# Optimization experiments

Hardware: AMD Instinct MI355X
Metric: run time of the kernel (lower is better)

The kernel has to match this reference:

```python
import jax, jax.numpy as jnp
import numpy as np

NUM_CLUSTERS = 64
DIM = 512
ALPHA = 100.0
EPS = 1e-12  # torch F.normalize eps


def setup_inputs() -> dict:
    key = jax.random.key(0)
    k1, k2 = jax.random.split(key)
    x1 = jax.random.normal(k1, (30, DIM, 28, 28), dtype=jnp.float32)
    centroids = jax.random.uniform(k2, (NUM_CLUSTERS, DIM), dtype=jnp.float32)
    # _init_params: conv weight = 2*alpha*centroids (1x1 conv), bias = -alpha*||centroid||
    conv_w = 2.0 * ALPHA * centroids
    conv_b = -ALPHA * jnp.linalg.norm(centroids, axis=1)
    return {"x1": x1, "centroids": centroids, "conv_w": conv_w, "conv_b": conv_b}


def _l2norm(v, axis):
    n = jnp.sqrt(jnp.sum(v * v, axis=axis, keepdims=True))
    return v / jnp.maximum(n, EPS)


def reference(x1, centroids, conv_w, conv_b):
    T, C, H, W = x1.shape
    K, D = centroids.shape
    x = x1.reshape(T, C, H * W)            # [T, C, N]
    x = _l2norm(x, axis=1)                 # normalize_input: L2 over channel dim
    # 1x1 conv == matmul over channels: logits [T, K, N]
    logits = jnp.einsum('kc,tcn->tkn', conv_w, x) + conv_b[None, :, None]
    a = jax.nn.softmax(logits, axis=1)     # soft assignment over clusters
    # vlad[t,k,c] = sum_n a[t,k,n]*(x[t,c,n] - centroids[k,c])
    # rewritten as two small matmuls, avoiding the [K,C,N] residual tensor
    vlad = jnp.einsum('tkn,tcn->tkc', a, x) - a.sum(axis=-1)[:, :, None] * centroids[None]
    vlad = _l2norm(vlad, axis=2)           # intra-normalization over feature dim
    v = vlad.reshape(T, K * D)
    v = _l2norm(v, axis=1)                 # global L2 normalization
    return v.sum(axis=0, keepdims=True)    # [1, K*D] accumulated over 30 timesteps
```

## Files before the change

kernel.cpp:

```cpp
#include <hip/hip_runtime.h>
#include <math.h>

#define T_ 30
#define C_ 512
#define N_ 784
#define NA_ 800
#define QP 36
#define EPSV 1e-12f

typedef __attribute__((ext_vector_type(8))) short bf16x8;
typedef __attribute__((ext_vector_type(4))) float f32x4;

__device__ __forceinline__ unsigned short f2bf(float f) {
    union { float f; unsigned int u; } v; v.f = f;
    unsigned int r = (v.u + 0x7FFFu + ((v.u >> 16) & 1u)) >> 16;
    return (unsigned short)r;
}
__device__ __forceinline__ float bf2f(unsigned short h) {
    union { unsigned int u; float f; } v; v.u = ((unsigned int)h) << 16;
    return v.f;
}

__global__ void k_prep(const float* __restrict__ w, unsigned short* __restrict__ wh,
                       unsigned short* __restrict__ wl) {
    int idx = blockIdx.x * 256 + threadIdx.x;
    float v = w[idx];
    unsigned short h = f2bf(v);
    wh[idx] = h;
    wl[idx] = f2bf(v - bf2f(h));
}

__global__ __launch_bounds__(256, 4) void k_assign(
    const float* __restrict__ x, const unsigned short* __restrict__ wh,
    const unsigned short* __restrict__ wl, const float* __restrict__ b,
    unsigned short* __restrict__ aT, float* __restrict__ asum)
{
    __shared__ __align__(16) char smem[4 * 32 * QP * 2 * 2];
    unsigned short* xh = (unsigned short*)smem;
    unsigned short* xl = xh + 4 * 32 * QP;
    float* red = (float*)smem;
    __shared__ float ssq[4][32];

    int t = blockIdx.y, n0 = blockIdx.x * 32;
    int tid = threadIdx.x;
    int w = tid >> 6, L = tid & 63, lid = L & 15, quad = L >> 4;
    int cbase = w * 128;
    int nseg = (L & 7) * 4;
    int crow = L >> 3;

    int ncol = n0 + nseg;
    if (ncol > 780) ncol = 780;
    const float* xb = x + (size_t)t * C_ * N_ + ncol;
    unsigned short* shh = xh + w * 32 * QP;
    unsigned short* shl = xl + w * 32 * QP;
    const unsigned short* wha = wh + (size_t)lid * C_ + cbase + quad * 8;
    const unsigned short* wla = wl + (size_t)lid * C_ + cbase + quad * 8;

    float bk = b[L];
    float ss0 = 0.f, ss1 = 0.f, ss2 = 0.f, ss3 = 0.f;
    f32x4 acc[4][2];
    #pragma unroll
    for (int mt = 0; mt < 4; ++mt)
        #pragma unroll
        for (int nt = 0; nt < 2; ++nt)
            #pragma unroll
            for (int r = 0; r < 4; ++r) acc[mt][nt][r] = 0.f;

    #pragma unroll
    for (int qtr = 0; qtr < 4; ++qtr) {
        float4 q[4];
        #pragma unroll
        for (int p = 0; p < 4; ++p)
            q[p] = *reinterpret_cast<const float4*>(
                xb + (size_t)(cbase + qtr * 32 + p * 8 + crow) * N_);
        #pragma unroll
        for (int p = 0; p < 4; ++p) {
            int cl = p * 8 + crow;
            float vv[4] = {q[p].x, q[p].y, q[p].z, q[p].w};
            ss0 = fmaf(vv[0], vv[0], ss0); ss1 = fmaf(vv[1], vv[1], ss1);
            ss2 = fmaf(vv[2], vv[2], ss2); ss3 = fmaf(vv[3], vv[3], ss3);
            #pragma unroll
            for (int j = 0; j < 4; ++j) {
                unsigned short h = f2bf(vv[j]);
                shh[(nseg + j) * QP + cl] = h;
                shl[(nseg + j) * QP + cl] = f2bf(vv[j] - bf2f(h));
            }
        }
        int so = quad * 8;
        bf16x8 bh0 = *reinterpret_cast<const bf16x8*>(&shh[lid * QP + so]);
        bf16x8 bl0 = *reinterpret_cast<const bf16x8*>(&shl[lid * QP + so]);
        bf16x8 bh1 = *reinterpret_cast<const bf16x8*>(&shh[(16 + lid) * QP + so]);
        bf16x8 bl1 = *reinterpret_cast<const bf16x8*>(&shl[(16 + lid) * QP + so]);
        int cg = qtr * 32;
        #pragma unroll
        for (int mt = 0; mt < 4; ++mt) {
            bf16x8 ah = *reinterpret_cast<const bf16x8*>(
                wha + (size_t)mt * 16 * C_ + cg);
            bf16x8 al = *reinterpret_cast<const bf16x8*>(
                wla + (size_t)mt * 16 * C_ + cg);
            acc[mt][0] = __builtin_amdgcn_mfma_f32_16x16x32_bf16(ah, bh0, acc[mt][0], 0, 0, 0);
            acc[mt][0] = __builtin_amdgcn_mfma_f32_16x16x32_bf16(al, bh0, acc[mt][0], 0, 0, 0);
            acc[mt][0] = __builtin_amdgcn_mfma_f32_16x16x32_bf16(ah, bl0, acc[mt][0], 0, 0, 0);
            acc[mt][1] = __builtin_amdgcn_mfma_f32_16x16x32_bf16(ah, bh1, acc[mt][1], 0, 0, 0);
            acc[mt][1] = __builtin_amdgcn_mfma_f32_16x16x32_bf16(al, bh1, acc[mt][1], 0, 0, 0);
            acc[mt][1] = __builtin_amdgcn_mfma_f32_16x16x32_bf16(ah, bl1, acc[mt][1], 0, 0, 0);
        }
    }
    #pragma unroll
    for (int m = 8; m <= 32; m <<= 1) {
        ss0 += __shfl_xor(ss0, m, 64); ss1 += __shfl_xor(ss1, m, 64);
        ss2 += __shfl_xor(ss2, m, 64); ss3 += __shfl_xor(ss3, m, 64);
    }
    if (L < 8) {
        ssq[w][L * 4 + 0] = ss0; ssq[w][L * 4 + 1] = ss1;
        ssq[w][L * 4 + 2] = ss2; ssq[w][L * 4 + 3] = ss3;
    }
    __syncthreads();

    float asl = 0.f;
    #pragma unroll
    for (int ph = 0; ph < 2; ++ph) {
        {
            float* rp = red + w * (16 * 68);
            #pragma unroll
            for (int mt = 0; mt < 4; ++mt)
                *reinterpret_cast<f32x4*>(&rp[lid * 68 + mt * 16 + quad * 4]) = acc[mt][ph];
        }
        __syncthreads();
        float vv[4], iv[4];
        #pragma unroll
        for (int i = 0; i < 4; ++i) {
            int nl = ph * 16 + w * 4 + i;
            float s = ssq[0][nl] + ssq[1][nl] + ssq[2][nl] + ssq[3][nl];
            iv[i] = 1.0f / fmaxf(sqrtf(s), EPSV);
            int nr = w * 4 + i;
            float v = red[0 * 1088 + nr * 68 + L] + red[1 * 1088 + nr * 68 + L]
                    + red[2 * 1088 + nr * 68 + L] + red[3 * 1088 + nr * 68 + L];
            vv[i] = fmaf(v, iv[i], bk);
        }
        float mx[4] = {vv[0], vv[1], vv[2], vv[3]};
        #pragma unroll
        for (int m = 1; m <= 32; m <<= 1) {
            #pragma unroll
            for (int i = 0; i < 4; ++i) mx[i] = fmaxf(mx[i], __shfl_xor(mx[i], m, 64));
        }
        float e[4], se[4];
        #pragma unroll
        for (int i = 0; i < 4; ++i) { e[i] = __expf(vv[i] - mx[i]); se[i] = e[i]; }
        #pragma unroll
        for (int m = 1; m <= 32; m <<= 1) {
            #pragma unroll
            for (int i = 0; i < 4; ++i) se[i] += __shfl_xor(se[i], m, 64);
        }
        unsigned short av[4];
        #pragma unroll
        for (int i = 0; i < 4; ++i) {
            bool valid = (n0 + ph * 16 + w * 4 + i) < N_;
            float a = e[i] / se[i];
            av[i] = valid ? f2bf(a * iv[i]) : (unsigned short)0;
            asl += valid ? a : 0.f;
        }
        ushort4 st; st.x = av[0]; st.y = av[1]; st.z = av[2]; st.w = av[3];
        *reinterpret_cast<ushort4*>(
            aT + ((size_t)t * 64 + L) * NA_ + n0 + ph * 16 + w * 4) = st;
        if (ph == 0) __syncthreads();
    }
    atomicAdd(&asum[t * 64 + L], asl);
}

__global__ __launch_bounds__(256, 4) void k_vlad(
    const float* __restrict__ x, const unsigned short* __restrict__ aT,
    const float* __restrict__ asum, const float* __restrict__ cent,
    float* __restrict__ vlad, float* __restrict__ g2)
{
    __shared__ float red[4][16 * 36];
    int t = blockIdx.z, kh = blockIdx.y, c0 = blockIdx.x * 16;
    int tid = threadIdx.x;
    int w = tid >> 6, L = tid & 63, lid = L & 15, quad = L >> 4;

    f32x4 acc[2];
    #pragma unroll
    for (int mt = 0; mt < 2; ++mt)
        #pragma unroll
        for (int r = 0; r < 4; ++r) acc[mt][r] = 0.f;

    const float* xrow = x + ((size_t)t * C_ + c0 + lid) * N_;
    const unsigned short* a0 = aT + ((size_t)t * 64 + kh * 32 + lid) * NA_;

    int k_loc = tid >> 3, j8 = tid & 7, ce = j8 * 2;
    int kg = kh * 32 + k_loc;
    float as = asum[t * 64 + kg];
    float2 cv = *reinterpret_cast<const float2*>(cent + kg * C_ + c0 + ce);

    int nb = w * 32 + quad * 8;
    int nc = nb > 776 ? 776 : nb;
    float4 x0c = *reinterpret_cast<const float4*>(xrow + nc);
    float4 x1c = *reinterpret_cast<const float4*>(xrow + nc + 4);
    bf16x8 f0 = *reinterpret_cast<const bf16x8*>(a0 + nb);
    bf16x8 f1 = *reinterpret_cast<const bf16x8*>(a0 + 16 * NA_ + nb);

    for (int s = w; s < 25; s += 4) {
        int sn = s + 4;
        float4 x0n = x0c, x1n = x1c;
        bf16x8 g0 = f0, g1 = f1;
        if (sn < 25) {
            int nb2 = sn * 32 + quad * 8;
            int nc2 = nb2 > 776 ? 776 : nb2;
            x0n = *reinterpret_cast<const float4*>(xrow + nc2);
            x1n = *reinterpret_cast<const float4*>(xrow + nc2 + 4);
            g0  = *reinterpret_cast<const bf16x8*>(a0 + nb2);
            g1  = *reinterpret_cast<const bf16x8*>(a0 + 16 * NA_ + nb2);
        }
        bf16x8 bb;
        bb[0] = (short)f2bf(x0c.x); bb[1] = (short)f2bf(x0c.y);
        bb[2] = (short)f2bf(x0c.z); bb[3] = (short)f2bf(x0c.w);
        bb[4] = (short)f2bf(x1c.x); bb[5] = (short)f2bf(x1c.y);
        bb[6] = (short)f2bf(x1c.z); bb[7] = (short)f2bf(x1c.w);
        acc[0] = __builtin_amdgcn_mfma_f32_16x16x32_bf16(f0, bb, acc[0], 0, 0, 0);
        acc[1] = __builtin_amdgcn_mfma_f32_16x16x32_bf16(f1, bb, acc[1], 0, 0, 0);
        x0c = x0n; x1c = x1n; f0 = g0; f1 = g1;
    }
    {
        float* rp = &red[w][0];
        #pragma unroll
        for (int mt = 0; mt < 2; ++mt)
            *reinterpret_cast<f32x4*>(&rp[lid * 36 + mt * 16 + quad * 4]) = acc[mt];
    }
    __syncthreads();

    float2 vout;
    float s2 = 0.f;
    #pragma unroll
    for (int j = 0; j < 2; ++j) {
        int cc = ce + j;
        float v = red[0][cc * 36 + k_loc] + red[1][cc * 36 + k_loc]
                + red[2][cc * 36 + k_loc] + red[3][cc * 36 + k_loc];
        v -= as * ((const float*)&cv)[j];
        ((float*)&vout)[j] = v;
        s2 = fmaf(v, v, s2);
    }
    *reinterpret_cast<float2*>(vlad + ((size_t)t * 64 + kg) * C_ + c0 + ce) = vout;
    s2 += __shfl_xor(s2, 1, 64);
    s2 += __shfl_xor(s2, 2, 64);
    s2 += __shfl_xor(s2, 4, 64);
    if (j8 == 0) atomicAdd(&g2[t * 64 + kg], s2);
}

__global__ __launch_bounds__(256) void k_out(
    const float* __restrict__ vlad, const float* __restrict__ g2,
    float* __restrict__ out)
{
    __shared__ float intr[1920];
    __shared__ float gl[1920];
    __shared__ float sinv[T_];
    __shared__ float part[256];
    int tid = threadIdx.x;
    for (int i = tid; i < 1920; i += 256) {
        float s = g2[i];
        gl[i] = s;
        intr[i] = 1.0f / fmaxf(sqrtf(s), EPSV);
    }
    __syncthreads();
    if (tid < T_) {
        float s = 0.f;
        #pragma unroll 8
        for (int k = 0; k < 64; ++k) {
            float iv = intr[tid * 64 + k];
            s += gl[tid * 64 + k] * iv * iv;
        }
        sinv[tid] = 1.0f / fmaxf(sqrtf(s), EPSV);
    }
    __syncthreads();
    int idx = blockIdx.x * 128 + (tid & 127);
    int th = tid >> 7;
    int k = idx >> 9;
    float s = 0.f;
    #pragma unroll
    for (int t = th * 15; t < th * 15 + 15; ++t)
        s += vlad[(size_t)t * 32768 + idx] * intr[t * 64 + k] * sinv[t];
    part[tid] = s;
    __syncthreads();
    if (tid < 128) out[idx] = part[tid] + part[tid + 128];
}

extern "C" void kernel_launch(void* const* d_in, const int* in_sizes, int n_in,
                              void* d_out, int out_size, void* d_ws, size_t ws_size,
                              hipStream_t stream) {
    const float* x    = (const float*)d_in[0];
    const float* cent = (const float*)d_in[1];
    const float* w    = (const float*)d_in[2];
    const float* b    = (const float*)d_in[3];
    float* out = (float*)d_out;

    char* p = (char*)d_ws;
    unsigned short* wh = (unsigned short*)p;  p += 65536;
    unsigned short* wl = (unsigned short*)p;  p += 65536;
    float* asum = (float*)p;                  p += 1920 * 4;
    float* g2   = (float*)p;                  p += 1920 * 4;
    float* vlad = (float*)p;                  p += (size_t)T_ * 64 * C_ * 4;
    unsigned short* aT = (unsigned short*)p;  p += (size_t)T_ * 64 * NA_ * 2;

    k_prep<<<128, 256, 0, stream>>>(w, wh, wl);
    hipMemsetAsync(asum, 0, 2 * 1920 * 4, stream);
    k_assign<<<dim3(25, T_), 256, 0, stream>>>(x, wh, wl, b, aT, asum);
    k_vlad<<<dim3(32, 2, T_), 256, 0, stream>>>(x, aT, asum, cent, vlad, g2);
    k_out<<<256, 256, 0, stream>>>(vlad, g2, out);
}
```

Before: 130.2 us.

## Split assignment GEMM over channel halves and combine softmax in separate kernel

The assignment kernel is split along the channel dimension into two halves, which doubles the grid from 750 to 1500 blocks. Each half writes partial logits and partial squared norms to workspace. A new combine kernel sums the partials, then applies normalization, bias and softmax, writes aT with coalesced 16-byte stores, and accumulates asum. The goal is more parallelism and occupancy in the GEMM stage. The cost is an extra kernel launch and a round trip of partial logits through global memory.

```diff
diff --git a/kernel.cpp b/kernel.cpp
--- a/kernel.cpp
+++ b/kernel.cpp
@@ -30,10 +30,10 @@
     wl[idx] = f2bf(v - bf2f(h));
 }
 
-__global__ __launch_bounds__(256, 4) void k_assign(
+__global__ __launch_bounds__(256, 4) void k_assign_p(
     const float* __restrict__ x, const unsigned short* __restrict__ wh,
-    const unsigned short* __restrict__ wl, const float* __restrict__ b,
-    unsigned short* __restrict__ aT, float* __restrict__ asum)
+    const unsigned short* __restrict__ wl,
+    float* __restrict__ plog, float* __restrict__ pssq)
 {
     __shared__ __align__(16) char smem[4 * 32 * QP * 2 * 2];
     unsigned short* xh = (unsigned short*)smem;
@@ -41,10 +41,11 @@
     float* red = (float*)smem;
     __shared__ float ssq[4][32];
 
-    int t = blockIdx.y, n0 = blockIdx.x * 32;
+    int bx = blockIdx.x, ch = blockIdx.y, t = blockIdx.z;
+    int n0 = bx * 32;
     int tid = threadIdx.x;
     int w = tid >> 6, L = tid & 63, lid = L & 15, quad = L >> 4;
-    int cbase = w * 128;
+    int cbase = ch * 256 + w * 64;
     int nseg = (L & 7) * 4;
     int crow = L >> 3;
 
@@ -56,7 +57,6 @@
     const unsigned short* wha = wh + (size_t)lid * C_ + cbase + quad * 8;
     const unsigned short* wla = wl + (size_t)lid * C_ + cbase + quad * 8;
 
-    float bk = b[L];
     float ss0 = 0.f, ss1 = 0.f, ss2 = 0.f, ss3 = 0.f;
     f32x4 acc[4][2];
     #pragma unroll
@@ -67,7 +67,7 @@
             for (int r = 0; r < 4; ++r) acc[mt][nt][r] = 0.f;
 
     #pragma unroll
-    for (int qtr = 0; qtr < 4; ++qtr) {
+    for (int qtr = 0; qtr < 2; ++qtr) {
         float4 q[4];
         #pragma unroll
         for (int p = 0; p < 4; ++p)
@@ -117,7 +117,12 @@
     }
     __syncthreads();
 
-    float asl = 0.f;
+    if (tid < 32) {
+        float s = ssq[0][tid] + ssq[1][tid] + ssq[2][tid] + ssq[3][tid];
+        pssq[(size_t)(ch * 30 + t) * 800 + n0 + tid] = s;
+    }
+
+    float* pl = plog + (size_t)((ch * 30 + t) * 25 + bx) * 2048;
     #pragma unroll
     for (int ph = 0; ph < 2; ++ph) {
         {
@@ -127,45 +132,71 @@
                 *reinterpret_cast<f32x4*>(&rp[lid * 68 + mt * 16 + quad * 4]) = acc[mt][ph];
         }
         __syncthreads();
-        float vv[4], iv[4];
         #pragma unroll
         for (int i = 0; i < 4; ++i) {
-            int nl = ph * 16 + w * 4 + i;
-            float s = ssq[0][nl] + ssq[1][nl] + ssq[2][nl] + ssq[3][nl];
-            iv[i] = 1.0f / fmaxf(sqrtf(s), EPSV);
             int nr = w * 4 + i;
             float v = red[0 * 1088 + nr * 68 + L] + red[1 * 1088 + nr * 68 + L]
                     + red[2 * 1088 + nr * 68 + L] + red[3 * 1088 + nr * 68 + L];
-            vv[i] = fmaf(v, iv[i], bk);
-        }
-        float mx[4] = {vv[0], vv[1], vv[2], vv[3]};
-        #pragma unroll
-        for (int m = 1; m <= 32; m <<= 1) {
-            #pragma unroll
-            for (int i = 0; i < 4; ++i) mx[i] = fmaxf(mx[i], __shfl_xor(mx[i], m, 64));
-        }
-        float e[4], se[4];
-        #pragma unroll
-        for (int i = 0; i < 4; ++i) { e[i] = __expf(vv[i] - mx[i]); se[i] = e[i]; }
-        #pragma unroll
-        for (int m = 1; m <= 32; m <<= 1) {
-            #pragma unroll
-            for (int i = 0; i < 4; ++i) se[i] += __shfl_xor(se[i], m, 64);
-        }
-        unsigned short av[4];
-        #pragma unroll
-        for (int i = 0; i < 4; ++i) {
-            bool valid = (n0 + ph * 16 + w * 4 + i) < N_;
-            float a = e[i] / se[i];
-            av[i] = valid ? f2bf(a * iv[i]) : (unsigned short)0;
-            asl += valid ? a : 0.f;
-        }
-        ushort4 st; st.x = av[0]; st.y = av[1]; st.z = av[2]; st.w = av[3];
-        *reinterpret_cast<ushort4*>(
-            aT + ((size_t)t * 64 + L) * NA_ + n0 + ph * 16 + w * 4) = st;
+            pl[(ph * 16 + nr) * 64 + L] = v;
+        }
         if (ph == 0) __syncthreads();
     }
+}
+
+__global__ __launch_bounds__(256) void k_cmb(
+    const float* __restrict__ plog, const float* __restrict__ pssq,
+    const float* __restrict__ b, unsigned short* __restrict__ aT,
+    float* __restrict__ asum)
+{
+    __shared__ unsigned short atl[64][40];
+    int bx = blockIdx.x, t = blockIdx.y, n0 = bx * 32;
+    int tid = threadIdx.x, w = tid >> 6, L = tid & 63;
+
+    const float* p0 = plog + (size_t)((0 * 30 + t) * 25 + bx) * 2048;
+    const float* p1 = plog + (size_t)((1 * 30 + t) * 25 + bx) * 2048;
+    const float* s0 = pssq + (size_t)(0 * 30 + t) * 800 + n0;
+    const float* s1 = pssq + (size_t)(1 * 30 + t) * 800 + n0;
+    float bk = b[L];
+
+    float vv[8], iv[8];
+    #pragma unroll
+    for (int i = 0; i < 8; ++i) {
+        int nl = w * 8 + i;
+        float s = s0[nl] + s1[nl];
+        iv[i] = 1.0f / fmaxf(sqrtf(s), EPSV);
+        float v = p0[nl * 64 + L] + p1[nl * 64 + L];
+        vv[i] = fmaf(v, iv[i], bk);
+    }
+    float mx[8];
+    #pragma unroll
+    for (int i = 0; i < 8; ++i) mx[i] = vv[i];
+    #pragma unroll
+    for (int m = 1; m <= 32; m <<= 1) {
+        #pragma unroll
+        for (int i = 0; i < 8; ++i) mx[i] = fmaxf(mx[i], __shfl_xor(mx[i], m, 64));
+    }
+    float e[8], se[8];
+    #pragma unroll
+    for (int i = 0; i < 8; ++i) { e[i] = __expf(vv[i] - mx[i]); se[i] = e[i]; }
+    #pragma unroll
+    for (int m = 1; m <= 32; m <<= 1) {
+        #pragma unroll
+        for (int i = 0; i < 8; ++i) se[i] += __shfl_xor(se[i], m, 64);
+    }
+    float asl = 0.f;
+    #pragma unroll
+    for (int i = 0; i < 8; ++i) {
+        int nl = w * 8 + i;
+        bool valid = (n0 + nl) < N_;
+        float a = e[i] / se[i];
+        atl[L][nl] = valid ? f2bf(a * iv[i]) : (unsigned short)0;
+        asl += valid ? a : 0.f;
+    }
     atomicAdd(&asum[t * 64 + L], asl);
+    __syncthreads();
+    int k = tid >> 2, ng = tid & 3;
+    uint4 ov = *reinterpret_cast<const uint4*>(&atl[k][ng * 8]);
+    *reinterpret_cast<uint4*>(aT + ((size_t)t * 64 + k) * NA_ + n0 + ng * 8) = ov;
 }
 
 __global__ __launch_bounds__(256, 4) void k_vlad(
@@ -299,10 +330,13 @@
     float* g2   = (float*)p;                  p += 1920 * 4;
     float* vlad = (float*)p;                  p += (size_t)T_ * 64 * C_ * 4;
     unsigned short* aT = (unsigned short*)p;  p += (size_t)T_ * 64 * NA_ * 2;
+    float* plog = (float*)p;                  p += (size_t)2 * T_ * 25 * 2048 * 4;
+    float* pssq = (float*)p;                  p += (size_t)2 * T_ * 800 * 4;
 
     k_prep<<<128, 256, 0, stream>>>(w, wh, wl);
     hipMemsetAsync(asum, 0, 2 * 1920 * 4, stream);
-    k_assign<<<dim3(25, T_), 256, 0, stream>>>(x, wh, wl, b, aT, asum);
+    k_assign_p<<<dim3(25, 2, T_), 256, 0, stream>>>(x, wh, wl, plog, pssq);
+    k_cmb<<<dim3(25, T_), 256, 0, stream>>>(plog, pssq, b, aT, asum);
     k_vlad<<<dim3(32, 2, T_), 256, 0, stream>>>(x, aT, asum, cent, vlad, g2);
     k_out<<<256, 256, 0, stream>>>(vlad, g2, out);
 }
```

Measured after the change: 140.1 us. 1.08x slower.
